# Kernel optimization log

Hardware: AMD Instinct MI355X
Metric: run time of the kernel (lower is better)

The kernel has to match this reference:

```python
import jax, jax.numpy as jnp
import numpy as np
from jax import lax

DN = ('NCHW', 'OIHW', 'NCHW')


def setup_inputs() -> dict:
    key = jax.random.key(0)
    ks = jax.random.split(key, 5)
    B, C, H, W = 32, 512, 56, 56
    R = 16
    return {
        'x': jax.random.normal(ks[0], (B, C, H, W), jnp.float32),
        'w1': jax.random.normal(ks[1], (1, 3, 3, 3), jnp.float32) * 0.2,   # shared conv over (y1,y2,y4) triplet
        'w2': jax.random.normal(ks[2], (1, 1, 3, 3), jnp.float32) * 0.2,   # shared depthwise conv
        'fc1_w': jax.random.normal(ks[3], (C // R, C), jnp.float32) * 0.05,
        'fc2_w': jax.random.normal(ks[4], (C, C // R), jnp.float32) * 0.05,
    }


def reference(x, w1, w2, fc1_w, fc2_w):
    b, c, h, w = x.shape
    # multi-scale adaptive average pooling (H,W divisible by 4) + nearest upsample to 4x4
    y1 = jnp.broadcast_to(x.mean(axis=(2, 3), keepdims=True), (b, c, 4, 4))      # pool1 -> interp x4
    y2 = x.reshape(b, c, 2, h // 2, 2, w // 2).mean(axis=(3, 5))                 # [b,c,2,2]
    y2 = jnp.repeat(jnp.repeat(y2, 2, axis=2), 2, axis=3)                        # nearest interp x2 -> 4x4
    y4 = x.reshape(b, c, 4, h // 4, 4, w // 4).mean(axis=(3, 5))                 # [b,c,4,4]
    # ShareGroupConv(3c->c): out channel j sees channels (j, c+j, 2c+j) = (y1_j, y2_j, y4_j)
    t = jnp.stack([y1, y2, y4], axis=2).reshape(b * c, 3, 4, 4)
    z = lax.conv_general_dilated(t, w1, (1, 1), 'VALID', dimension_numbers=DN)   # [b*c,1,2,2]
    # ShareGroupConv(c->c, k=3, pad=1, stride=3): shared per-channel conv, 2x2 -> 1x1
    z = lax.conv_general_dilated(z, w2, (3, 3), [(1, 1), (1, 1)], dimension_numbers=DN)
    s = z.reshape(b, c)
    s = jax.nn.relu(s @ fc1_w.T) @ fc2_w.T
    s = jax.nn.sigmoid(s).reshape(b, c, 1, 1)
    return x * s
```

## Files before the change

### kernel.cpp

```cpp
#include <hip/hip_runtime.h>
#include <math.h>

#define Bn 32
#define Cn 512
#define Hn 56
#define Wn 56
#define HW (Hn*Wn)
#define NPLANE (Bn*Cn)
#define F4_PER_PLANE (HW/4)

typedef float f4 __attribute__((ext_vector_type(4)));

__global__ __launch_bounds__(256) void pool_conv_kernel(
    const float* __restrict__ x,
    const float* __restrict__ w1,
    const float* __restrict__ w2,
    float* __restrict__ s0)
{
    __shared__ float plane[HW];
    __shared__ float rs[Hn * 4];
    __shared__ float y4[16];

    const int bc = blockIdx.x;
    const int t  = threadIdx.x;
    const float* src = x + (size_t)bc * HW;

    for (int f = t; f < F4_PER_PLANE; f += 256)
        ((f4*)plane)[f] = ((const f4*)src)[f];
    __syncthreads();

    if (t < Hn * 4) {
        const int h = t >> 2, j = t & 3;
        const float* row = plane + h * Wn + j * 14;
        float s = 0.f;
        #pragma unroll
        for (int e = 0; e < 14; ++e) s += row[e];
        rs[h * 4 + j] = s;
    }
    __syncthreads();

    if (t < 16) {
        const int i = t >> 2, j = t & 3;
        float s = 0.f;
        #pragma unroll
        for (int r = 0; r < 14; ++r) s += rs[(i * 14 + r) * 4 + j];
        y4[i * 4 + j] = s * (1.0f / 196.0f);
    }
    __syncthreads();

    if (t == 0) {
        float y2[2][2];
        #pragma unroll
        for (int p = 0; p < 2; ++p)
            #pragma unroll
            for (int q = 0; q < 2; ++q)
                y2[p][q] = 0.25f * (y4[(2*p)*4 + 2*q]   + y4[(2*p)*4 + 2*q+1]
                                  + y4[(2*p+1)*4 + 2*q] + y4[(2*p+1)*4 + 2*q+1]);
        const float y1 = 0.25f * (y2[0][0] + y2[0][1] + y2[1][0] + y2[1][1]);

        float z[2][2];
        #pragma unroll
        for (int oy = 0; oy < 2; ++oy)
            #pragma unroll
            for (int ox = 0; ox < 2; ++ox) {
                float acc = 0.f;
                #pragma unroll
                for (int ky = 0; ky < 3; ++ky)
                    #pragma unroll
                    for (int kx = 0; kx < 3; ++kx) {
                        const int yy = oy + ky, xx = ox + kx;
                        acc += y1                   * w1[0*9 + ky*3 + kx];
                        acc += y2[yy >> 1][xx >> 1] * w1[1*9 + ky*3 + kx];
                        acc += y4[yy*4 + xx]        * w1[2*9 + ky*3 + kx];
                    }
                z[oy][ox] = acc;
            }

        s0[bc] = z[0][0] * w2[1*3+1] + z[0][1] * w2[1*3+2]
               + z[1][0] * w2[2*3+1] + z[1][1] * w2[2*3+2];
    }
}

__global__ __launch_bounds__(256) void fc_scale_kernel(
    const float* __restrict__ x,
    const float* __restrict__ s0,
    const float* __restrict__ fc1,
    const float* __restrict__ fc2,
    float* __restrict__ out)
{
    __shared__ float sv[Cn];
    __shared__ float hv[32];
    __shared__ float scl[8];

    const int b  = blockIdx.x >> 6;
    const int kk = blockIdx.x & 63;
    const int t  = threadIdx.x;

    for (int c = t; c < Cn; c += 256) sv[c] = s0[b * Cn + c];
    __syncthreads();

    {
        const int r = t >> 3, lane8 = t & 7;
        float acc = 0.f;
        for (int c = lane8; c < Cn; c += 8) acc += sv[c] * fc1[r * Cn + c];
        acc += __shfl_xor(acc, 1);
        acc += __shfl_xor(acc, 2);
        acc += __shfl_xor(acc, 4);
        if (lane8 == 0) hv[r] = fmaxf(acc, 0.f);
    }
    __syncthreads();

    if (t < 8) {
        const int c = kk * 8 + t;
        float acc = 0.f;
        #pragma unroll
        for (int r = 0; r < 32; ++r) acc += hv[r] * fc2[c * 32 + r];
        scl[t] = 1.0f / (1.0f + expf(-acc));
    }
    __syncthreads();

    #pragma unroll
    for (int p = 0; p < 8; ++p) {
        const int plane = b * Cn + kk * 8 + p;
        const float sc = scl[p];
        const f4* px = (const f4*)x + (size_t)plane * F4_PER_PLANE;
        f4* po = (f4*)out + (size_t)plane * F4_PER_PLANE;
        for (int f = t; f < F4_PER_PLANE; f += 256) {
            f4 v = px[f];
            v *= sc;
            __builtin_nontemporal_store(v, po + f);
        }
    }
}

extern "C" void kernel_launch(void* const* d_in, const int* in_sizes, int n_in,
                              void* d_out, int out_size, void* d_ws, size_t ws_size,
                              hipStream_t stream) {
    const float* x   = (const float*)d_in[0];
    const float* w1  = (const float*)d_in[1];
    const float* w2  = (const float*)d_in[2];
    const float* fc1 = (const float*)d_in[3];
    const float* fc2 = (const float*)d_in[4];
    float* out = (float*)d_out;

    float* s0 = (float*)d_ws;

    pool_conv_kernel<<<NPLANE, 256, 0, stream>>>(x, w1, w2, s0);
    fc_scale_kernel<<<Bn * 64, 256, 0, stream>>>(x, s0, fc1, fc2, out);
}
```

Baseline: 108.1 us.

## Split pool and scale kernels into batch chunks for L2/MALL reuse of x

Launches pool and scale kernels alternately over four batch chunks instead of once over the full tensor. Each chunk's x (about 51 MB) is meant to still sit in the last-level cache when the scale kernel rereads it, so the second read of x comes less often from HBM. In exchange there are eight launches instead of two, and each launch has a smaller grid with fill and drain tails at every boundary.

```diff
diff --git a/kernel.cpp b/kernel.cpp
--- a/kernel.cpp
+++ b/kernel.cpp
@@ -7,7 +7,11 @@
 #define Wn 56
 #define HW (Hn*Wn)
 #define NPLANE (Bn*Cn)
-#define F4_PER_PLANE (HW/4)
+#define F4P (HW/4)
+
+#define NCHUNK 4
+#define BPC (Bn/NCHUNK)
+#define PPC (BPC*Cn)
 
 typedef float f4 __attribute__((ext_vector_type(4)));
 
@@ -15,17 +19,18 @@
     const float* __restrict__ x,
     const float* __restrict__ w1,
     const float* __restrict__ w2,
-    float* __restrict__ s0)
+    float* __restrict__ s0,
+    int off)
 {
     __shared__ float plane[HW];
     __shared__ float rs[Hn * 4];
     __shared__ float y4[16];
 
-    const int bc = blockIdx.x;
+    const int bc = off + blockIdx.x;
     const int t  = threadIdx.x;
     const float* src = x + (size_t)bc * HW;
 
-    for (int f = t; f < F4_PER_PLANE; f += 256)
+    for (int f = t; f < F4P; f += 256)
         ((f4*)plane)[f] = ((const f4*)src)[f];
     __syncthreads();
 
@@ -86,13 +91,14 @@
     const float* __restrict__ s0,
     const float* __restrict__ fc1,
     const float* __restrict__ fc2,
-    float* __restrict__ out)
+    float* __restrict__ out,
+    int batch_off)
 {
     __shared__ float sv[Cn];
     __shared__ float hv[32];
     __shared__ float scl[8];
 
-    const int b  = blockIdx.x >> 6;
+    const int b  = batch_off + (blockIdx.x >> 6);
     const int kk = blockIdx.x & 63;
     const int t  = threadIdx.x;
 
@@ -100,13 +106,13 @@
     __syncthreads();
 
     {
-        const int r = t >> 3, lane8 = t & 7;
+        const int r = t >> 3, l8 = t & 7;
         float acc = 0.f;
-        for (int c = lane8; c < Cn; c += 8) acc += sv[c] * fc1[r * Cn + c];
+        for (int c = l8; c < Cn; c += 8) acc += sv[c] * fc1[r * Cn + c];
         acc += __shfl_xor(acc, 1);
         acc += __shfl_xor(acc, 2);
         acc += __shfl_xor(acc, 4);
-        if (lane8 == 0) hv[r] = fmaxf(acc, 0.f);
+        if (l8 == 0) hv[r] = fmaxf(acc, 0.f);
     }
     __syncthreads();
 
@@ -123,9 +129,9 @@
     for (int p = 0; p < 8; ++p) {
         const int plane = b * Cn + kk * 8 + p;
         const float sc = scl[p];
-        const f4* px = (const f4*)x + (size_t)plane * F4_PER_PLANE;
-        f4* po = (f4*)out + (size_t)plane * F4_PER_PLANE;
-        for (int f = t; f < F4_PER_PLANE; f += 256) {
+        const f4* px = (const f4*)x   + (size_t)plane * F4P;
+        f4*       po = (f4*)out      + (size_t)plane * F4P;
+        for (int f = t; f < F4P; f += 256) {
             f4 v = px[f];
             v *= sc;
             __builtin_nontemporal_store(v, po + f);
@@ -142,9 +148,11 @@
     const float* fc1 = (const float*)d_in[3];
     const float* fc2 = (const float*)d_in[4];
     float* out = (float*)d_out;
+    float* s0  = (float*)d_ws;
 
-    float* s0 = (float*)d_ws;
-
-    pool_conv_kernel<<<NPLANE, 256, 0, stream>>>(x, w1, w2, s0);
-    fc_scale_kernel<<<Bn * 64, 256, 0, stream>>>(x, s0, fc1, fc2, out);
+    for (int c = 0; c < NCHUNK; ++c) {
+        pool_conv_kernel<<<PPC, 256, 0, stream>>>(x, w1, w2, s0, c * PPC);
+        fc_scale_kernel<<<BPC * 64, 256, 0, stream>>>(x, s0, fc1, fc2, out,
+                                                      c * BPC);
+    }
 }
```

Measured after the change: 148.1 us. +37.1%, slower.
